# Performance work log

Hardware: AMD Instinct MI355X
Metric: run time of the kernel (lower is better)

The kernel has to match this reference:

```python
import jax, jax.numpy as jnp
import numpy as np

M, N, K = 1024, 11008, 4096


def _unpack_i2u(Bp):
    """Unpack 2-bit unsigned weights per decode_i2u_to_i8s interleave.

    Bp: [N, K//4] int8 storage. Within each group of 4 bytes (16 elements),
    output element at position 4*i + j = (byte_j >> (2*i)) & 3.
    Returns [N, K] int8 with values in {0,1,2,3}.
    """
    Bu = jax.lax.bitcast_convert_type(Bp, jnp.uint8)  # [N, K//4]
    n, kc = Bu.shape
    Bg = Bu.reshape(n, kc // 4, 1, 4)                 # [N, G, 1, j]
    shifts = (jnp.arange(4, dtype=jnp.uint8) * jnp.uint8(2)).reshape(1, 1, 4, 1)
    vals = (Bg >> shifts) & jnp.uint8(3)              # [N, G, i, j]
    return vals.reshape(n, kc * 4).astype(jnp.int8)   # [N, K]


def setup_inputs() -> dict:
    key = jax.random.key(0)
    k1, k2 = jax.random.split(key)
    A = jax.random.randint(k1, (M, K), -128, 128, dtype=jnp.int8)
    B = jax.random.randint(k2, (N, K // 4), -128, 128, dtype=jnp.int8)
    return {"A": A, "B": B}


def reference(A, B):
    W = _unpack_i2u(B)  # [N, K] int8
    C = jax.lax.dot_general(
        A, W,
        dimension_numbers=(((1,), (1,)), ((), ())),
        preferred_element_type=jnp.int32,
    )  # [M, N] int32
    return C
```

## Files before the change

kernel.cpp:

```cpp
#include <hip/hip_runtime.h>
#include <stdint.h>


#define MM 1024
#define NN 11008
#define KK 4096
#define KSTEPS (KK / 64)
#define MTILES (MM / 128)
#define NTILES (NN / 128)

using i32x4  = __attribute__((ext_vector_type(4))) int;
using i32x16 = __attribute__((ext_vector_type(16))) int;

__device__ __forceinline__ int pack4(i32x4 v) {
    return (int)(((uint32_t)v[0] & 0xFFu) | (((uint32_t)v[1] & 0xFFu) << 8)
               | (((uint32_t)v[2] & 0xFFu) << 16) | (((uint32_t)v[3] & 0xFFu) << 24));
}

__global__ __launch_bounds__(256) void prep_A(const int* __restrict__ src,
                                              uint8_t* __restrict__ dst) {
    const int g = blockIdx.x * 256 + threadIdx.x;
    const int kstep = g >> 12;
    const int rem   = g & 4095;
    const int mtile = rem >> 9;
    const int c     = rem & 511;
    const int wr  = (c >> 8) & 1, mi = (c >> 7) & 1, kk2 = (c >> 6) & 1;
    const int lane = c & 63;
    const int row   = mtile * 128 + wr * 64 + mi * 32 + (lane & 31);
    const int kbyte = kstep * 64 + kk2 * 32 + (lane >> 5) * 16;
    const i32x4* s4 = (const i32x4*)(src + (size_t)row * KK + kbyte);
    i32x4 o;
#pragma unroll
    for (int q = 0; q < 4; ++q) o[q] = pack4(s4[q]);
    *(i32x4*)(dst + (size_t)g * 16) = o;
}

__global__ __launch_bounds__(256) void prep_B(const int* __restrict__ src,
                                              uint8_t* __restrict__ dst) {
    const int t = blockIdx.x * 256 + threadIdx.x;
    const int kstep = t / (NTILES * 128);
    const int rem   = t % (NTILES * 128);
    const int ntile = rem >> 7;
    const int c     = rem & 127;
    const int d0    = c * 4;
    const int wc  = (d0 >> 8) & 1, ni = (d0 >> 7) & 1, kk2 = (d0 >> 6) & 1;
    const int j   = kk2 * 2 + ((d0 & 63) >> 5);
    const int n0  = ntile * 128 + wc * 64 + ni * 32 + (d0 & 31);
    i32x4 o;
#pragma unroll
    for (int q = 0; q < 4; ++q) {
        const i32x4 v = *(const i32x4*)(src + (size_t)(n0 + q) * (KK / 4) + kstep * 16 + j * 4);
        o[q] = pack4(v);
    }
    *(i32x4*)(dst + (size_t)t * 16) = o;
}

#define GLOAD_LDS16(g, l) __builtin_amdgcn_global_load_lds(                    \
        (const __attribute__((address_space(1))) uint32_t*)(g),                \
        (__attribute__((address_space(3))) uint32_t*)(l), 16, 0, 0)

__global__ __launch_bounds__(256) void bitnet_gemm(const uint8_t* __restrict__ A2,
                                                   const uint8_t* __restrict__ B2,
                                                   int* __restrict__ C) {
    const int t    = threadIdx.x;
    const int lane = t & 63, wave = t >> 6;
    const int wr   = wave >> 1, wc = wave & 1;
    const int l31  = lane & 31, h = lane >> 5;
    const int by   = blockIdx.y, bx = blockIdx.x;

    __shared__ __align__(16) uint8_t As[2][8192];
    __shared__ __align__(16) uint8_t Bs[2][2048];

    i32x16 acc[2][2] = {};

    auto STAGE = [&](int buf, int ks) {
        const uint8_t* at = A2 + ((size_t)ks * MTILES + by) * 8192;
        GLOAD_LDS16(at + t * 16,        &As[buf][wave * 1024]);
        GLOAD_LDS16(at + 4096 + t * 16, &As[buf][4096 + wave * 1024]);
        if (wave < 2) {
            const uint8_t* bt = B2 + ((size_t)ks * NTILES + bx) * 2048;
            GLOAD_LDS16(bt + t * 16, &Bs[buf][wave * 1024]);
        }
    };

    auto COMPUTE = [&](int buf) {
        const uint8_t* ab = As[buf];
        const uint8_t* bb = Bs[buf];
#pragma unroll
        for (int kk2 = 0; kk2 < 2; ++kk2) {
            i32x4 a0 = *(const i32x4*)(ab + ((wr * 2 + 0) * 2 + kk2) * 1024 + lane * 16);
            i32x4 a1 = *(const i32x4*)(ab + ((wr * 2 + 1) * 2 + kk2) * 1024 + lane * 16);
            const uint32_t p0 = *(const uint32_t*)(bb + ((wc * 2 + 0) * 2 + kk2) * 256 + lane * 4);
            const uint32_t p1 = *(const uint32_t*)(bb + ((wc * 2 + 1) * 2 + kk2) * 256 + lane * 4);
            i32x4 b0, b1;
#pragma unroll
            for (int i = 0; i < 4; ++i) {
                b0[i] = (int)((p0 >> (2 * i)) & 0x03030303u);
                b1[i] = (int)((p1 >> (2 * i)) & 0x03030303u);
            }
            acc[0][0] = __builtin_amdgcn_mfma_i32_32x32x32_i8(a0, b0, acc[0][0], 0, 0, 0);
            acc[0][1] = __builtin_amdgcn_mfma_i32_32x32x32_i8(a0, b1, acc[0][1], 0, 0, 0);
            acc[1][0] = __builtin_amdgcn_mfma_i32_32x32x32_i8(a1, b0, acc[1][0], 0, 0, 0);
            acc[1][1] = __builtin_amdgcn_mfma_i32_32x32x32_i8(a1, b1, acc[1][1], 0, 0, 0);
        }
    };

    STAGE(0, 0);
    __syncthreads();

#pragma unroll 1
    for (int ks = 0; ks < KSTEPS - 2; ks += 2) {
        STAGE(1, ks + 1);
        COMPUTE(0);
        __syncthreads();
        STAGE(0, ks + 2);
        COMPUTE(1);
        __syncthreads();
    }
    STAGE(1, KSTEPS - 1);
    COMPUTE(0);
    __syncthreads();
    COMPUTE(1);

    const int brow = by * 128, bcol = bx * 128;
#pragma unroll
    for (int mi = 0; mi < 2; ++mi)
#pragma unroll
        for (int ni = 0; ni < 2; ++ni) {
            const int colg = bcol + wc * 64 + ni * 32 + l31;
#pragma unroll
            for (int r = 0; r < 16; ++r) {
                const int rowin = (r & 3) + 8 * (r >> 2) + 4 * h;
                const int rowg  = brow + wr * 64 + mi * 32 + rowin;
                C[(size_t)rowg * NN + colg] = acc[mi][ni][r];
            }
        }
}

extern "C" void kernel_launch(void* const* d_in, const int* in_sizes, int n_in,
                              void* d_out, int out_size, void* d_ws, size_t ws_size,
                              hipStream_t stream) {
    const int* A32 = (const int*)d_in[0];
    const int* B32 = (const int*)d_in[1];
    int* C = (int*)d_out;

    uint8_t* A2 = (uint8_t*)d_ws;
    uint8_t* B2 = A2 + (size_t)MM * KK;

    prep_A<<<dim3((MM * KK / 16) / 256), dim3(256), 0, stream>>>(A32, A2);
    prep_B<<<dim3((NN * 64) / 256), dim3(256), 0, stream>>>(B32, B2);
    bitnet_gemm<<<dim3(NTILES, MTILES), dim3(256), 0, stream>>>(A2, B2, C);
}
```

Before: 75.96 us.

## Replace LDS staging with direct register loads from MFMA-ready global layout

The GEMM no longer stages A and B tiles through shared memory with global_load_lds and barriers. Each wave now loads its MFMA operand fragments straight from global memory into registers, double-buffered across k-steps, and the B prep layout is reshuffled so each lane reads one 16-byte vector per k-step. A launch-bounds occupancy hint is also added. This removes the LDS round trip and the __syncthreads calls, but the waves of a block no longer share A and B fragments, so cache traffic rises and latency hiding depends on register double-buffering and occupancy.

```diff
diff --git a/kernel.cpp b/kernel.cpp
--- a/kernel.cpp
+++ b/kernel.cpp
@@ -5,7 +5,7 @@
 #define MM 1024
 #define NN 11008
 #define KK 4096
-#define KSTEPS (KK / 64)
+#define KSTEPS 64
 #define MTILES (MM / 128)
 #define NTILES (NN / 128)
 
@@ -24,9 +24,9 @@
     const int rem   = g & 4095;
     const int mtile = rem >> 9;
     const int c     = rem & 511;
-    const int wr  = (c >> 8) & 1, mi = (c >> 7) & 1, kk2 = (c >> 6) & 1;
-    const int lane = c & 63;
-    const int row   = mtile * 128 + wr * 64 + mi * 32 + (lane & 31);
+    const int row32 = (c >> 7) & 3, kk2 = (c >> 6) & 1;
+    const int lane  = c & 63;
+    const int row   = mtile * 128 + row32 * 32 + (lane & 31);
     const int kbyte = kstep * 64 + kk2 * 32 + (lane >> 5) * 16;
     const i32x4* s4 = (const i32x4*)(src + (size_t)row * KK + kbyte);
     i32x4 o;
@@ -38,89 +38,83 @@
 __global__ __launch_bounds__(256) void prep_B(const int* __restrict__ src,
                                               uint8_t* __restrict__ dst) {
     const int t = blockIdx.x * 256 + threadIdx.x;
-    const int kstep = t / (NTILES * 128);
-    const int rem   = t % (NTILES * 128);
-    const int ntile = rem >> 7;
-    const int c     = rem & 127;
-    const int d0    = c * 4;
-    const int wc  = (d0 >> 8) & 1, ni = (d0 >> 7) & 1, kk2 = (d0 >> 6) & 1;
-    const int j   = kk2 * 2 + ((d0 & 63) >> 5);
-    const int n0  = ntile * 128 + wc * 64 + ni * 32 + (d0 & 31);
+    const int lane = t & 63;
+    const int wc   = (t >> 6) & 1;
+    const int rem  = t >> 7;
+    const int ntile = rem % NTILES;
+    const int kstep = rem / NTILES;
+    const int l31 = lane & 31, h = lane >> 5;
     i32x4 o;
 #pragma unroll
     for (int q = 0; q < 4; ++q) {
-        const i32x4 v = *(const i32x4*)(src + (size_t)(n0 + q) * (KK / 4) + kstep * 16 + j * 4);
+        const int ni = q >> 1, kk2 = q & 1;
+        const int n  = ntile * 128 + wc * 64 + ni * 32 + l31;
+        const i32x4 v = *(const i32x4*)(src + (size_t)n * (KK / 4) + kstep * 16 + kk2 * 8 + h * 4);
         o[q] = pack4(v);
     }
     *(i32x4*)(dst + (size_t)t * 16) = o;
 }
 
-#define GLOAD_LDS16(g, l) __builtin_amdgcn_global_load_lds(                    \
-        (const __attribute__((address_space(1))) uint32_t*)(g),                \
-        (__attribute__((address_space(3))) uint32_t*)(l), 16, 0, 0)
-
-__global__ __launch_bounds__(256) void bitnet_gemm(const uint8_t* __restrict__ A2,
-                                                   const uint8_t* __restrict__ B2,
-                                                   int* __restrict__ C) {
+__global__ __launch_bounds__(256, 3) void bitnet_gemm(const uint8_t* __restrict__ A2,
+                                                      const uint8_t* __restrict__ B3,
+                                                      int* __restrict__ C) {
     const int t    = threadIdx.x;
     const int lane = t & 63, wave = t >> 6;
     const int wr   = wave >> 1, wc = wave & 1;
     const int l31  = lane & 31, h = lane >> 5;
     const int by   = blockIdx.y, bx = blockIdx.x;
 
-    __shared__ __align__(16) uint8_t As[2][8192];
-    __shared__ __align__(16) uint8_t Bs[2][2048];
+    const size_t strideA = (size_t)MTILES * 8192;
+    const size_t strideB = (size_t)NTILES * 2048;
+
+    const uint8_t* pa[4];
+#pragma unroll
+    for (int s = 0; s < 4; ++s) {
+        const int mi = s >> 1, kk2 = s & 1;
+        pa[s] = A2 + (size_t)by * 8192 + ((wr * 2 + mi) * 2 + kk2) * 1024 + lane * 16;
+    }
+    const uint8_t* pb = B3 + (size_t)bx * 2048 + wc * 1024 + lane * 16;
 
     i32x16 acc[2][2] = {};
+    i32x4 a0[4], a1[4], p0, p1;
 
-    auto STAGE = [&](int buf, int ks) {
-        const uint8_t* at = A2 + ((size_t)ks * MTILES + by) * 8192;
-        GLOAD_LDS16(at + t * 16,        &As[buf][wave * 1024]);
-        GLOAD_LDS16(at + 4096 + t * 16, &As[buf][4096 + wave * 1024]);
-        if (wave < 2) {
-            const uint8_t* bt = B2 + ((size_t)ks * NTILES + bx) * 2048;
-            GLOAD_LDS16(bt + t * 16, &Bs[buf][wave * 1024]);
+    auto LOAD = [&](i32x4 (&a)[4], i32x4& p, int ks) {
+#pragma unroll
+        for (int s = 0; s < 4; ++s)
+            a[s] = *(const i32x4*)(pa[s] + (size_t)ks * strideA);
+        p = *(const i32x4*)(pb + (size_t)ks * strideB);
+    };
+
+    auto COMPUTE = [&](const i32x4 (&a)[4], const i32x4& p) {
+#pragma unroll
+        for (int kk2 = 0; kk2 < 2; ++kk2) {
+            const uint32_t q0 = (uint32_t)p[kk2];
+            const uint32_t q1 = (uint32_t)p[2 + kk2];
+            i32x4 b0, b1;
+#pragma unroll
+            for (int i = 0; i < 4; ++i) {
+                b0[i] = (int)((q0 >> (2 * i)) & 0x03030303u);
+                b1[i] = (int)((q1 >> (2 * i)) & 0x03030303u);
+            }
+            acc[0][0] = __builtin_amdgcn_mfma_i32_32x32x32_i8(a[0 * 2 + kk2], b0, acc[0][0], 0, 0, 0);
+            acc[0][1] = __builtin_amdgcn_mfma_i32_32x32x32_i8(a[0 * 2 + kk2], b1, acc[0][1], 0, 0, 0);
+            acc[1][0] = __builtin_amdgcn_mfma_i32_32x32x32_i8(a[1 * 2 + kk2], b0, acc[1][0], 0, 0, 0);
+            acc[1][1] = __builtin_amdgcn_mfma_i32_32x32x32_i8(a[1 * 2 + kk2], b1, acc[1][1], 0, 0, 0);
         }
     };
 
-    auto COMPUTE = [&](int buf) {
-        const uint8_t* ab = As[buf];
-        const uint8_t* bb = Bs[buf];
-#pragma unroll
-        for (int kk2 = 0; kk2 < 2; ++kk2) {
-            i32x4 a0 = *(const i32x4*)(ab + ((wr * 2 + 0) * 2 + kk2) * 1024 + lane * 16);
-            i32x4 a1 = *(const i32x4*)(ab + ((wr * 2 + 1) * 2 + kk2) * 1024 + lane * 16);
-            const uint32_t p0 = *(const uint32_t*)(bb + ((wc * 2 + 0) * 2 + kk2) * 256 + lane * 4);
-            const uint32_t p1 = *(const uint32_t*)(bb + ((wc * 2 + 1) * 2 + kk2) * 256 + lane * 4);
-            i32x4 b0, b1;
-#pragma unroll
-            for (int i = 0; i < 4; ++i) {
-                b0[i] = (int)((p0 >> (2 * i)) & 0x03030303u);
-                b1[i] = (int)((p1 >> (2 * i)) & 0x03030303u);
-            }
-            acc[0][0] = __builtin_amdgcn_mfma_i32_32x32x32_i8(a0, b0, acc[0][0], 0, 0, 0);
-            acc[0][1] = __builtin_amdgcn_mfma_i32_32x32x32_i8(a0, b1, acc[0][1], 0, 0, 0);
-            acc[1][0] = __builtin_amdgcn_mfma_i32_32x32x32_i8(a1, b0, acc[1][0], 0, 0, 0);
-            acc[1][1] = __builtin_amdgcn_mfma_i32_32x32x32_i8(a1, b1, acc[1][1], 0, 0, 0);
-        }
-    };
-
-    STAGE(0, 0);
-    __syncthreads();
+    LOAD(a0, p0, 0);
+    LOAD(a1, p1, 1);
 
 #pragma unroll 1
     for (int ks = 0; ks < KSTEPS - 2; ks += 2) {
-        STAGE(1, ks + 1);
-        COMPUTE(0);
-        __syncthreads();
-        STAGE(0, ks + 2);
-        COMPUTE(1);
-        __syncthreads();
+        COMPUTE(a0, p0);
+        LOAD(a0, p0, ks + 2);
+        COMPUTE(a1, p1);
+        LOAD(a1, p1, ks + 3);
     }
-    STAGE(1, KSTEPS - 1);
-    COMPUTE(0);
-    __syncthreads();
-    COMPUTE(1);
+    COMPUTE(a0, p0);
+    COMPUTE(a1, p1);
 
     const int brow = by * 128, bcol = bx * 128;
 #pragma unroll
@@ -145,9 +139,9 @@
     int* C = (int*)d_out;
 
     uint8_t* A2 = (uint8_t*)d_ws;
-    uint8_t* B2 = A2 + (size_t)MM * KK;
+    uint8_t* B3 = A2 + (size_t)MM * KK;
 
     prep_A<<<dim3((MM * KK / 16) / 256), dim3(256), 0, stream>>>(A32, A2);
-    prep_B<<<dim3((NN * 64) / 256), dim3(256), 0, stream>>>(B32, B2);
-    bitnet_gemm<<<dim3(NTILES, MTILES), dim3(256), 0, stream>>>(A2, B2, C);
+    prep_B<<<dim3((NN * 64) / 256), dim3(256), 0, stream>>>(B32, B3);
+    bitnet_gemm<<<dim3(NTILES, MTILES), dim3(256), 0, stream>>>(A2, B3, C);
 }
```

Result: faster. 73.53 us (-3.2%).
